# Performance work log

Measured on AMD Instinct MI355X. Metric: run time of the kernel, lower is better.

## Reference

```python
import jax, jax.numpy as jnp
import numpy as np

B, N, DIM = 4, 16384, 512
H, D, S = 8, 64, 64  # heads, dim_head, n_global_queries
SCALE = 1.0  # FLARE hardcodes scale=1.0


def setup_inputs() -> dict:
    key = jax.random.key(0)
    ks = jax.random.split(key, 10)
    inner = H * D
    s = 0.02
    return {
        "x": jax.random.normal(ks[0], (B, N, DIM), dtype=jnp.float32),
        "q_global": jax.random.normal(ks[1], (1, H, S, D), dtype=jnp.float32),
        "Wx": jax.random.normal(ks[2], (DIM, inner), dtype=jnp.float32) * s,
        "bx": jnp.zeros((inner,), dtype=jnp.float32),
        "Wk": jax.random.normal(ks[3], (D, D), dtype=jnp.float32) * s,
        "bk": jnp.zeros((D,), dtype=jnp.float32),
        "Wv": jax.random.normal(ks[4], (D, D), dtype=jnp.float32) * s,
        "bv": jnp.zeros((D,), dtype=jnp.float32),
        "Wo": jax.random.normal(ks[5], (inner, DIM), dtype=jnp.float32) * s,
        "bo": jnp.zeros((DIM,), dtype=jnp.float32),
    }


def reference(x, q_global, Wx, bx, Wk, bk, Wv, bv, Wo, bo):
    b, n, c = x.shape
    # input projection + split heads: B N (H D) -> B H N D
    x_mid = (x @ Wx + bx).reshape(b, n, H, D).transpose(0, 2, 1, 3)
    # per-head k/v projections (dim_head x dim_head)
    k = x_mid @ Wk + bk  # [B,H,N,D]
    v = x_mid @ Wv + bv  # [B,H,N,D]
    G = q_global  # broadcast over batch
    # pass 1: aggregate tokens into S global slots
    attn1 = jax.nn.softmax(jnp.einsum('bhsd,bhnd->bhsn', jnp.broadcast_to(G, (b, H, S, D)), k) * SCALE, axis=-1)
    z = jnp.einsum('bhsn,bhnd->bhsd', attn1, v)  # [B,H,S,D]
    # pass 2: distribute slots back to tokens (query=k, key=G, value=z)
    attn2 = jax.nn.softmax(jnp.einsum('bhnd,bhsd->bhns', k, jnp.broadcast_to(G, (b, H, S, D))) * SCALE, axis=-1)
    y = jnp.einsum('bhns,bhsd->bhnd', attn2, z)  # [B,H,N,D]
    # merge heads + output projection
    out = y.transpose(0, 2, 1, 3).reshape(b, n, H * D)
    return out @ Wo + bo
```

## Files before the change

kernel.cpp:

```cpp
#include <hip/hip_runtime.h>
#include <stdint.h>

#define DEV __device__ __forceinline__

typedef __attribute__((ext_vector_type(8))) short bf16x8;
typedef __attribute__((ext_vector_type(4))) float f32x4;
typedef __attribute__((ext_vector_type(8))) unsigned short u16x8;

DEV unsigned short f2bf(float f) {
  union { float f; unsigned int u; } v; v.f = f;
  unsigned int u = v.u;
  return (unsigned short)((u + 0x7FFFu + ((u >> 16) & 1u)) >> 16);
}
DEV float bf2f(unsigned short u) {
  union { unsigned int u; float f; } v; v.u = ((unsigned int)u) << 16;
  return v.f;
}
DEV f32x4 mfma16(bf16x8 a, bf16x8 b, f32x4 c) {
  return __builtin_amdgcn_mfma_f32_16x16x32_bf16(a, b, c, 0, 0, 0);
}
DEV void gl_lds16(const void* g, void* l) {
  __builtin_amdgcn_global_load_lds(
      (const __attribute__((address_space(1))) void*)g,
      (__attribute__((address_space(3))) void*)l, 16, 0, 0);
}

__global__ __launch_bounds__(256) void k_misc1(const float* __restrict__ x,
                                               unsigned short* __restrict__ xbf,
                                               const float* __restrict__ Wk,
                                               const float* __restrict__ qg,
                                               float* __restrict__ GK) {
  int bid = blockIdx.x;
  if (bid < 16384) {
    int i = bid * 256 + threadIdx.x;
    const float4* p = (const float4*)x + (size_t)i * 2;
    float4 a = p[0], b = p[1];
    u16x8 o;
    o[0] = f2bf(a.x); o[1] = f2bf(a.y); o[2] = f2bf(a.z); o[3] = f2bf(a.w);
    o[4] = f2bf(b.x); o[5] = f2bf(b.y); o[6] = f2bf(b.z); o[7] = f2bf(b.w);
    ((u16x8*)xbf)[i] = o;
  } else {
    int idx = (bid - 16384) * 256 + threadIdx.x;
    int dd = idx & 63, hs = idx >> 6;
    float a = 0.f;
#pragma unroll 8
    for (int d = 0; d < 64; ++d) a += Wk[dd * 64 + d] * qg[(size_t)hs * 64 + d];
    GK[idx] = a;
  }
}

__global__ __launch_bounds__(256) void k_misc2(const float* __restrict__ Wx,
                                               const float* __restrict__ Wv,
                                               const float* __restrict__ Wo,
                                               const float* __restrict__ bx,
                                               const float* __restrict__ bk,
                                               const float* __restrict__ bv,
                                               const float* __restrict__ qg,
                                               const float* __restrict__ GK,
                                               unsigned short* __restrict__ Wcat,
                                               unsigned short* __restrict__ WoT,
                                               float* __restrict__ bias) {
  int bid = blockIdx.x;
  if (bid < 1024) {
    int idx = bid * 256 + threadIdx.x;
    int c = idx & 511, hs = idx >> 9;
    int h = hs >> 6, s = hs & 63;
    float a = 0.f;
#pragma unroll 8
    for (int dd = 0; dd < 64; ++dd) a += Wx[(size_t)c * 512 + h * 64 + dd] * GK[hs * 64 + dd];
    Wcat[(size_t)(h * 128 + s) * 512 + c] = f2bf(a);
  } else if (bid < 2048) {
    int idx = (bid - 1024) * 256 + threadIdx.x;
    int c = idx & 511, o = idx >> 9;
    int h = o >> 6, dp = o & 63;
    float a = 0.f;
#pragma unroll 8
    for (int dd = 0; dd < 64; ++dd) a += Wx[(size_t)c * 512 + h * 64 + dd] * Wv[dd * 64 + dp];
    Wcat[(size_t)(h * 128 + 64 + dp) * 512 + c] = f2bf(a);
  } else if (bid < 3072) {
    int idx = (bid - 2048) * 256 + threadIdx.x;
    int i = idx >> 9, o = idx & 511;
    WoT[(size_t)o * 512 + i] = f2bf(Wo[(size_t)i * 512 + o]);
  } else {
    int o = (bid - 3072) * 256 + threadIdx.x;
    if (o >= 1024) return;
    int h = o >> 7, j = o & 127;
    if (j < 64) {
      int hs = h * 64 + j;
      float a = 0.f;
      for (int dd = 0; dd < 64; ++dd) a += bx[h * 64 + dd] * GK[(size_t)hs * 64 + dd];
      for (int dp = 0; dp < 64; ++dp) a += bk[dp] * qg[(size_t)hs * 64 + dp];
      bias[o] = a;
    } else {
      int dp = j - 64;
      float a = bv[dp];
      for (int dd = 0; dd < 64; ++dd) a += bx[h * 64 + dd] * Wv[dd * 64 + dp];
      bias[o] = a;
    }
  }
}

template <int MODE>
__global__ __launch_bounds__(256, 4) void k_mm(const unsigned short* __restrict__ A,
                                               const unsigned short* __restrict__ BTg,
                                               const float* __restrict__ bias,
                                               unsigned short* __restrict__ P2,
                                               float* __restrict__ zpart,
                                               float* __restrict__ dpart,
                                               float* __restrict__ outF) {
  __shared__ __align__(16) char lds[35328];
  const int tid = threadIdx.x;
  const int w = tid >> 6, lane = tid & 63, l = lane & 15, g = lane >> 4;
  unsigned bid = blockIdx.x;
  int mtile, ntile;
  if (MODE == 1) {
    unsigned nbid = (bid & 7) * 512 + (bid >> 3);
    mtile = nbid >> 3;
    ntile = nbid & 7;
  } else {
    unsigned nbid = (bid & 7) * 256 + (bid >> 3);
    mtile = nbid >> 2;
    ntile = nbid & 3;
  }
  const int bm = mtile * 128;
  const int bn = ntile * 128;
  const int b = mtile >> 7;
  const unsigned short* BT = (MODE == 0) ? BTg + ((size_t)b << 18) : BTg;
  const int wm = (w >> 1) * 64, wn = (w & 1) * 64;
  char* As = lds;
  char* Bs = lds + 16384;
  f32x4 acc[4][4] = {};
  const int sw = (l & 7) << 4;

  for (int t = 0; t < 8; ++t) {
#pragma unroll
    for (int i = 0; i < 4; ++i) {
      int off = i * 4096 + tid * 16;
      int row = off >> 7;
      int cb = (off & 127) ^ ((row & 7) << 4);
      gl_lds16(A + (size_t)(bm + row) * 512 + t * 64 + (cb >> 1), As + off);
      gl_lds16(BT + (size_t)(bn + row) * 512 + t * 64 + (cb >> 1), Bs + off);
    }
    __syncthreads();
#pragma unroll
    for (int ks = 0; ks < 2; ++ks) {
      int kb = (ks * 64 + g * 16) ^ sw;
      bf16x8 af[4], bf[4];
#pragma unroll
      for (int fm = 0; fm < 4; ++fm)
        af[fm] = *(const bf16x8*)(As + (wm + fm * 16 + l) * 128 + kb);
#pragma unroll
      for (int fn = 0; fn < 4; ++fn)
        bf[fn] = *(const bf16x8*)(Bs + (wn + fn * 16 + l) * 128 + kb);
#pragma unroll
      for (int fm = 0; fm < 4; ++fm)
#pragma unroll
        for (int fn = 0; fn < 4; ++fn)
          acc[fm][fn] = mfma16(af[fm], bf[fn], acc[fm][fn]);
    }
    __syncthreads();
  }

  if (MODE == 0) {
#pragma unroll
    for (int fm = 0; fm < 4; ++fm)
#pragma unroll
      for (int fn = 0; fn < 4; ++fn) {
        int col = bn + wn + fn * 16 + l;
        float bb = bias[col];
#pragma unroll
        for (int r = 0; r < 4; ++r)
          outF[(size_t)(bm + wm + fm * 16 + g * 4 + r) * 512 + col] = acc[fm][fn][r] + bb;
      }
    return;
  }

  const int h = ntile;
  unsigned short* ET = (unsigned short*)lds;
  unsigned short* VT = (unsigned short*)(lds + 17408);
  float* denp = (float*)(lds + 34816);
  float bc[4];
#pragma unroll
  for (int fn = 0; fn < 4; ++fn) bc[fn] = bias[h * 128 + wn + fn * 16 + l];
  if (wn == 0) {
#pragma unroll
    for (int fm = 0; fm < 4; ++fm)
#pragma unroll
      for (int fn = 0; fn < 4; ++fn)
#pragma unroll
        for (int r = 0; r < 4; ++r)
          acc[fm][fn][r] = __expf(acc[fm][fn][r] + bc[fn] - 8.0f);
#pragma unroll
    for (int fm = 0; fm < 4; ++fm) {
      f32x4 rs;
#pragma unroll
      for (int r = 0; r < 4; ++r) {
        float t2 = (acc[fm][0][r] + acc[fm][1][r]) + (acc[fm][2][r] + acc[fm][3][r]);
#pragma unroll
        for (int m = 1; m < 16; m <<= 1) t2 += __shfl_xor(t2, m);
        rs[r] = t2;
      }
#pragma unroll
      for (int r = 0; r < 4; ++r) {
        float rinv = 1.f / rs[r];
        int n = bm + wm + fm * 16 + g * 4 + r;
#pragma unroll
        for (int fn = 0; fn < 4; ++fn)
          P2[(size_t)n * 512 + h * 64 + fn * 16 + l] = f2bf(acc[fm][fn][r] * rinv);
      }
    }
#pragma unroll
    for (int fm = 0; fm < 4; ++fm)
#pragma unroll
      for (int fn = 0; fn < 4; ++fn)
#pragma unroll
        for (int r = 0; r < 4; ++r)
          ET[(fn * 16 + l) * 136 + wm + fm * 16 + g * 4 + r] = f2bf(acc[fm][fn][r]);
#pragma unroll
    for (int fn = 0; fn < 4; ++fn) {
      float t2 = 0.f;
#pragma unroll
      for (int fm = 0; fm < 4; ++fm)
#pragma unroll
        for (int r = 0; r < 4; ++r) t2 += acc[fm][fn][r];
      t2 += __shfl_xor(t2, 16);
      t2 += __shfl_xor(t2, 32);
      if (g == 0) denp[(w >> 1) * 64 + fn * 16 + l] = t2;
    }
  } else {
#pragma unroll
    for (int fm = 0; fm < 4; ++fm)
#pragma unroll
      for (int fn = 0; fn < 4; ++fn)
#pragma unroll
        for (int r = 0; r < 4; ++r)
          VT[(fn * 16 + l) * 136 + wm + fm * 16 + g * 4 + r] =
              f2bf(acc[fm][fn][r] + bc[fn]);
  }
  __syncthreads();
  f32x4 za[4] = {};
#pragma unroll
  for (int ks2 = 0; ks2 < 4; ++ks2) {
    bf16x8 a2 = *(const bf16x8*)&ET[(w * 16 + l) * 136 + ks2 * 32 + g * 8];
#pragma unroll
    for (int fd = 0; fd < 4; ++fd) {
      bf16x8 b2 = *(const bf16x8*)&VT[(fd * 16 + l) * 136 + ks2 * 32 + g * 8];
      za[fd] = mfma16(a2, b2, za[fd]);
    }
  }
  size_t mh = (size_t)mtile * 8 + h;
#pragma unroll
  for (int fd = 0; fd < 4; ++fd)
#pragma unroll
    for (int r = 0; r < 4; ++r)
      zpart[mh * 4096 + (w * 16 + g * 4 + r) * 64 + fd * 16 + l] = za[fd][r];
  if (w == 0) dpart[mh * 64 + lane] = denp[lane] + denp[64 + lane];
}

__global__ void k_zred(const float* __restrict__ zpart, const float* __restrict__ dpart,
                       float* __restrict__ z) {
  int idx = blockIdx.x * 256 + threadIdx.x;
  int bh = idx >> 12, s = (idx >> 6) & 63, d = idx & 63;
  int b = bh >> 3, h = bh & 7;
  float num = 0.f, den = 0.f;
  for (int mm = 0; mm < 128; ++mm) {
    size_t mh = ((size_t)(b * 128 + mm)) * 8 + h;
    num += zpart[mh * 4096 + s * 64 + d];
    den += dpart[mh * 64 + s];
  }
  z[idx] = num / den;
}

__global__ void k_zwo(const float* __restrict__ z, const unsigned short* __restrict__ WoT,
                      unsigned short* __restrict__ zWoT) {
  int idx = blockIdx.x * 256 + threadIdx.x;
  int hs = idx & 511, c = (idx >> 9) & 511, b = idx >> 18;
  int h = hs >> 6;
  const float* zp = z + ((size_t)(b * 8 + h) * 64 + (hs & 63)) * 64;
  const unsigned short* wp = WoT + (size_t)c * 512 + h * 64;
  float a = 0.f;
#pragma unroll 8
  for (int d = 0; d < 64; ++d) a += zp[d] * bf2f(wp[d]);
  zWoT[((size_t)(b * 512) + c) * 512 + hs] = f2bf(a);
}

extern "C" void kernel_launch(void* const* d_in, const int* in_sizes, int n_in,
                              void* d_out, int out_size, void* d_ws, size_t ws_size,
                              hipStream_t stream) {
  const float* x  = (const float*)d_in[0];
  const float* qg = (const float*)d_in[1];
  const float* Wx = (const float*)d_in[2];
  const float* bx = (const float*)d_in[3];
  const float* Wk = (const float*)d_in[4];
  const float* bk = (const float*)d_in[5];
  const float* Wv = (const float*)d_in[6];
  const float* bv = (const float*)d_in[7];
  const float* Wo = (const float*)d_in[8];
  const float* bo = (const float*)d_in[9];
  float* out = (float*)d_out;

  char* ws = (char*)d_ws;
  unsigned short* xbf  = (unsigned short*)(ws);
  unsigned short* P2   = (unsigned short*)(ws + 67108864);
  unsigned short* Wcat = (unsigned short*)(ws + 134217728);
  unsigned short* WoT  = (unsigned short*)(ws + 135266304);
  float* bias          = (float*)(ws + 135790592);
  float* GK            = (float*)(ws + 135794688);
  unsigned short* zWoT = (unsigned short*)(ws + 135925760);
  float* zbuf          = (float*)(ws + 138027008);
  char* dob = (char*)d_out;
  float* zpart = (float*)(dob);
  float* dpart = (float*)(dob + 67108864);

  k_misc1<<<dim3(16512), dim3(256), 0, stream>>>(x, xbf, Wk, qg, GK);
  k_misc2<<<dim3(3076), dim3(256), 0, stream>>>(Wx, Wv, Wo, bx, bk, bv, qg, GK,
                                                Wcat, WoT, bias);
  k_mm<1><<<dim3(4096), dim3(256), 0, stream>>>(xbf, Wcat, bias, P2, zpart, dpart, nullptr);
  k_zred<<<dim3(512), dim3(256), 0, stream>>>(zpart, dpart, zbuf);
  k_zwo<<<dim3(4096), dim3(256), 0, stream>>>(zbuf, WoT, zWoT);
  k_mm<0><<<dim3(2048), dim3(256), 0, stream>>>(P2, zWoT, bo, nullptr, nullptr, nullptr, out);
}
```

Baseline: 262.2 us.

## Fuse x bf16 conversion into first GEMM loads and merge prep kernels

Removes the separate pass that converts x to bf16 in workspace. The first GEMM now reads fp32 x directly, converts it with packed cvt instructions and stores it into LDS. This replaces the async global-to-LDS load on the A side. The GK precompute is folded into the weight-prep kernel via shared memory, which drops one launch and its buffer. The trade-off is that the GEMM's A loads become synchronous register round trips of twice the bytes. Because each x row is read by 8 N-tiles, fp32 traffic into the GEMM grows, although L2 may absorb much of it.

```diff
diff --git a/kernel.cpp b/kernel.cpp
--- a/kernel.cpp
+++ b/kernel.cpp
@@ -24,53 +24,42 @@
       (const __attribute__((address_space(1))) void*)g,
       (__attribute__((address_space(3))) void*)l, 16, 0, 0);
 }
-
-__global__ __launch_bounds__(256) void k_misc1(const float* __restrict__ x,
-                                               unsigned short* __restrict__ xbf,
-                                               const float* __restrict__ Wk,
-                                               const float* __restrict__ qg,
-                                               float* __restrict__ GK) {
-  int bid = blockIdx.x;
-  if (bid < 16384) {
-    int i = bid * 256 + threadIdx.x;
-    const float4* p = (const float4*)x + (size_t)i * 2;
-    float4 a = p[0], b = p[1];
-    u16x8 o;
-    o[0] = f2bf(a.x); o[1] = f2bf(a.y); o[2] = f2bf(a.z); o[3] = f2bf(a.w);
-    o[4] = f2bf(b.x); o[5] = f2bf(b.y); o[6] = f2bf(b.z); o[7] = f2bf(b.w);
-    ((u16x8*)xbf)[i] = o;
-  } else {
-    int idx = (bid - 16384) * 256 + threadIdx.x;
-    int dd = idx & 63, hs = idx >> 6;
+DEV unsigned cvtpk(float lo, float hi) {
+  unsigned r;
+  asm("v_cvt_pk_bf16_f32 %0, %1, %2" : "=v"(r) : "v"(lo), "v"(hi));
+  return r;
+}
+
+__global__ __launch_bounds__(256) void k_prep(const float* __restrict__ Wx,
+                                              const float* __restrict__ Wk,
+                                              const float* __restrict__ Wv,
+                                              const float* __restrict__ Wo,
+                                              const float* __restrict__ bx,
+                                              const float* __restrict__ bk,
+                                              const float* __restrict__ bv,
+                                              const float* __restrict__ qg,
+                                              unsigned short* __restrict__ Wcat,
+                                              unsigned short* __restrict__ WoT,
+                                              float* __restrict__ bias) {
+  __shared__ float gkrow[64];
+  int bid = blockIdx.x, tid = threadIdx.x;
+  if (bid < 1024) {
+    int idx = bid * 256 + tid;
+    int c = idx & 511, hs = idx >> 9;
+    int h = hs >> 6, s = hs & 63;
+    if (tid < 64) {
+      float a = 0.f;
+#pragma unroll 8
+      for (int d = 0; d < 64; ++d) a += Wk[tid * 64 + d] * qg[(size_t)hs * 64 + d];
+      gkrow[tid] = a;
+    }
+    __syncthreads();
     float a = 0.f;
 #pragma unroll 8
-    for (int d = 0; d < 64; ++d) a += Wk[dd * 64 + d] * qg[(size_t)hs * 64 + d];
-    GK[idx] = a;
-  }
-}
-
-__global__ __launch_bounds__(256) void k_misc2(const float* __restrict__ Wx,
-                                               const float* __restrict__ Wv,
-                                               const float* __restrict__ Wo,
-                                               const float* __restrict__ bx,
-                                               const float* __restrict__ bk,
-                                               const float* __restrict__ bv,
-                                               const float* __restrict__ qg,
-                                               const float* __restrict__ GK,
-                                               unsigned short* __restrict__ Wcat,
-                                               unsigned short* __restrict__ WoT,
-                                               float* __restrict__ bias) {
-  int bid = blockIdx.x;
-  if (bid < 1024) {
-    int idx = bid * 256 + threadIdx.x;
-    int c = idx & 511, hs = idx >> 9;
-    int h = hs >> 6, s = hs & 63;
-    float a = 0.f;
-#pragma unroll 8
-    for (int dd = 0; dd < 64; ++dd) a += Wx[(size_t)c * 512 + h * 64 + dd] * GK[hs * 64 + dd];
+    for (int dd = 0; dd < 64; ++dd) a += Wx[(size_t)c * 512 + h * 64 + dd] * gkrow[dd];
     Wcat[(size_t)(h * 128 + s) * 512 + c] = f2bf(a);
   } else if (bid < 2048) {
-    int idx = (bid - 1024) * 256 + threadIdx.x;
+    int idx = (bid - 1024) * 256 + tid;
     int c = idx & 511, o = idx >> 9;
     int h = o >> 6, dp = o & 63;
     float a = 0.f;
@@ -78,17 +67,21 @@
     for (int dd = 0; dd < 64; ++dd) a += Wx[(size_t)c * 512 + h * 64 + dd] * Wv[dd * 64 + dp];
     Wcat[(size_t)(h * 128 + 64 + dp) * 512 + c] = f2bf(a);
   } else if (bid < 3072) {
-    int idx = (bid - 2048) * 256 + threadIdx.x;
+    int idx = (bid - 2048) * 256 + tid;
     int i = idx >> 9, o = idx & 511;
     WoT[(size_t)o * 512 + i] = f2bf(Wo[(size_t)i * 512 + o]);
   } else {
-    int o = (bid - 3072) * 256 + threadIdx.x;
+    int o = (bid - 3072) * 256 + tid;
     if (o >= 1024) return;
     int h = o >> 7, j = o & 127;
     if (j < 64) {
       int hs = h * 64 + j;
       float a = 0.f;
-      for (int dd = 0; dd < 64; ++dd) a += bx[h * 64 + dd] * GK[(size_t)hs * 64 + dd];
+      for (int dd = 0; dd < 64; ++dd) {
+        float gk = 0.f;
+        for (int d = 0; d < 64; ++d) gk += Wk[dd * 64 + d] * qg[(size_t)hs * 64 + d];
+        a += bx[h * 64 + dd] * gk;
+      }
       for (int dp = 0; dp < 64; ++dp) a += bk[dp] * qg[(size_t)hs * 64 + dp];
       bias[o] = a;
     } else {
@@ -102,6 +95,7 @@
 
 template <int MODE>
 __global__ __launch_bounds__(256, 4) void k_mm(const unsigned short* __restrict__ A,
+                                               const float* __restrict__ Xf,
                                                const unsigned short* __restrict__ BTg,
                                                const float* __restrict__ bias,
                                                unsigned short* __restrict__ P2,
@@ -138,7 +132,19 @@
       int off = i * 4096 + tid * 16;
       int row = off >> 7;
       int cb = (off & 127) ^ ((row & 7) << 4);
-      gl_lds16(A + (size_t)(bm + row) * 512 + t * 64 + (cb >> 1), As + off);
+      if (MODE == 0) {
+        gl_lds16(A + (size_t)(bm + row) * 512 + t * 64 + (cb >> 1), As + off);
+      } else {
+        const float* src = Xf + (size_t)(bm + row) * 512 + t * 64 + (cb >> 1);
+        float4 lo = *(const float4*)src;
+        float4 hi = *(const float4*)(src + 4);
+        union { unsigned u[4]; u16x8 v; } pk;
+        pk.u[0] = cvtpk(lo.x, lo.y);
+        pk.u[1] = cvtpk(lo.z, lo.w);
+        pk.u[2] = cvtpk(hi.x, hi.y);
+        pk.u[3] = cvtpk(hi.z, hi.w);
+        *(u16x8*)(As + off) = pk.v;
+      }
       gl_lds16(BT + (size_t)(bn + row) * 512 + t * 64 + (cb >> 1), Bs + off);
     }
     __syncthreads();
@@ -300,23 +306,22 @@
   float* out = (float*)d_out;
 
   char* ws = (char*)d_ws;
-  unsigned short* xbf  = (unsigned short*)(ws);
-  unsigned short* P2   = (unsigned short*)(ws + 67108864);
-  unsigned short* Wcat = (unsigned short*)(ws + 134217728);
-  unsigned short* WoT  = (unsigned short*)(ws + 135266304);
-  float* bias          = (float*)(ws + 135790592);
-  float* GK            = (float*)(ws + 135794688);
-  unsigned short* zWoT = (unsigned short*)(ws + 135925760);
-  float* zbuf          = (float*)(ws + 138027008);
+  unsigned short* P2   = (unsigned short*)(ws);
+  unsigned short* Wcat = (unsigned short*)(ws + 67108864);
+  unsigned short* WoT  = (unsigned short*)(ws + 68157440);
+  float* bias          = (float*)(ws + 68681728);
+  unsigned short* zWoT = (unsigned short*)(ws + 68685824);
+  float* zbuf          = (float*)(ws + 70782976);
   char* dob = (char*)d_out;
   float* zpart = (float*)(dob);
   float* dpart = (float*)(dob + 67108864);
 
-  k_misc1<<<dim3(16512), dim3(256), 0, stream>>>(x, xbf, Wk, qg, GK);
-  k_misc2<<<dim3(3076), dim3(256), 0, stream>>>(Wx, Wv, Wo, bx, bk, bv, qg, GK,
-                                                Wcat, WoT, bias);
-  k_mm<1><<<dim3(4096), dim3(256), 0, stream>>>(xbf, Wcat, bias, P2, zpart, dpart, nullptr);
+  k_prep<<<dim3(3076), dim3(256), 0, stream>>>(Wx, Wk, Wv, Wo, bx, bk, bv, qg,
+                                               Wcat, WoT, bias);
+  k_mm<1><<<dim3(4096), dim3(256), 0, stream>>>(nullptr, x, Wcat, bias, P2, zpart,
+                                                dpart, nullptr);
   k_zred<<<dim3(512), dim3(256), 0, stream>>>(zpart, dpart, zbuf);
   k_zwo<<<dim3(4096), dim3(256), 0, stream>>>(zbuf, WoT, zWoT);
-  k_mm<0><<<dim3(2048), dim3(256), 0, stream>>>(P2, zWoT, bo, nullptr, nullptr, nullptr, out);
-}
+  k_mm<0><<<dim3(2048), dim3(256), 0, stream>>>(P2, nullptr, zWoT, bo, nullptr, nullptr,
+                                                nullptr, out);
+}
```

Result: slower. 324.1 us (+23.6%).
